# Optimization experiments

Hardware: AMD Instinct MI355X
Metric: run time of the kernel (lower is better)

Reference implementation:

```python
import jax, jax.numpy as jnp
import numpy as np

CHUNK = 64


def _rmsnorm(x, g, eps=1e-6):
    return x * jax.lax.rsqrt(jnp.mean(x * x, axis=-1, keepdims=True) + eps) * g


def setup_inputs() -> dict:
    key = jax.random.key(0)
    ks = jax.random.split(key, 8)
    B, L, D, N = 4, 4096, 512, 64
    s = 0.02
    return {
        'x': jax.random.normal(ks[0], (B, L, D), jnp.float32),
        'A_log': -jnp.ones((D,), jnp.float32) * jnp.log(2.0),
        'dt_bias': jnp.log(jnp.expm1(jax.random.uniform(ks[1], (D,), jnp.float32, 0.001, 0.1))),
        'D_skip': jnp.ones((D,), jnp.float32),
        'W_xproj': jax.random.normal(ks[2], (D, 2 * D), jnp.float32) * s,
        'b_xproj': jnp.zeros((2 * D,), jnp.float32),
        'W_B': jax.random.normal(ks[3], (D, N), jnp.float32) * s,
        'W_C': jax.random.normal(ks[4], (D, N), jnp.float32) * s,
        'W_dt': jax.random.normal(ks[5], (D, D), jnp.float32) * s,
        'g_Bnorm': jnp.ones((N,), jnp.float32),
        'g_Cnorm': jnp.ones((N,), jnp.float32),
        'g_outnorm': jnp.ones((D,), jnp.float32),
        'W_out': jax.random.normal(ks[6], (D, D), jnp.float32) * s,
        'b_out': jnp.zeros((D,), jnp.float32),
    }


def reference(x, A_log, dt_bias, D_skip, W_xproj, b_xproj, W_B, W_C, W_dt,
              g_Bnorm, g_Cnorm, g_outnorm, W_out, b_out):
    b, l, d = x.shape
    n = W_B.shape[1]
    p = CHUNK
    c = l // p  # L chosen divisible by chunk size (original pads otherwise)

    A = -jnp.exp(jnp.clip(A_log, -20.0, 2.0))  # (d,)
    xp = x @ W_xproj + b_xproj                  # (b,l,2d)
    x_bar, z = jnp.split(xp, 2, axis=-1)
    Bm = _rmsnorm(x_bar @ W_B, g_Bnorm)         # (b,l,n)
    Cm = _rmsnorm(x_bar @ W_C, g_Cnorm)         # (b,l,n)
    dt = jnp.clip(jax.nn.softplus(x_bar @ W_dt + dt_bias), 1e-4, 5.0)
    A_bar = jnp.exp(jnp.clip(dt * A, -20.0, 0.0))  # (b,l,d)

    to_chunks = lambda t: t.reshape(b, c, p, t.shape[-1]).transpose(1, 0, 2, 3)
    xc, Bc, Cc, Ac = map(to_chunks, (x_bar, Bm, Cm, A_bar))  # (c,b,p,*)
    mask = jnp.tril(jnp.ones((p, p), x.dtype))

    def process_chunk(prev_state, inputs):
        x_c, B_c, C_c, A_c = inputs
        log_a = jnp.log(jnp.clip(A_c, 1e-8, 1.0))
        la_cs = jnp.cumsum(log_a, axis=1)  # (b,p,d)
        # intra-chunk decay matrix M: (b,p,p,d)
        M = jnp.exp(la_cs[:, :, None, :] - la_cs[:, None, :, :]) * mask[None, :, :, None]
        BX = jnp.einsum('bpn,bpd->bpnd', B_c, x_c)
        state = jnp.einsum('bijd,bjnd->bind', M, BX)
        y_intra = jnp.einsum('bpn,bpnd->bpd', C_c, state)
        decay = jnp.exp(la_cs)
        y_inter = jnp.einsum('bpn,bpnd->bpd', C_c,
                             prev_state[:, None, :, :] * decay[:, :, None, :])
        y_c = y_intra + y_inter
        a_total = jnp.exp(la_cs[:, -1, :])             # (b,d)
        a_to_end = jnp.exp(la_cs[:, -1:, :] - la_cs)   # (b,p,d)
        chunk_state = jnp.einsum('bpn,bpd->bnd', B_c, x_c * a_to_end)
        new_state = prev_state * a_total[:, None, :] + chunk_state
        new_state = jnp.where(jnp.isfinite(new_state), new_state, 0.0)
        y_c = jnp.where(jnp.isfinite(y_c), y_c, 0.0)
        return new_state, y_c

    init = jnp.zeros((b, n, d), x.dtype)
    _, yc = jax.lax.scan(jax.checkpoint(process_chunk), init, (xc, Bc, Cc, Ac))
    y = yc.transpose(1, 0, 2, 3).reshape(b, l, d)
    y = jnp.where(jnp.isfinite(y), y, 0.0)
    y = y + D_skip * x_bar
    y = _rmsnorm(y, g_outnorm) * jax.nn.silu(z)
    return y @ W_out + b_out
```

## Files before the change

kernel.cpp:

```cpp
#include <hip/hip_runtime.h>
#include <hip/hip_bf16.h>
#include <math.h>

typedef __hip_bfloat16 bf16;
typedef __attribute__((ext_vector_type(8))) short short8;
typedef __attribute__((ext_vector_type(4))) float floatx4;

#define B_ 4
#define L_ 4096
#define D_ 512
#define M_ (B_*L_)

__device__ __forceinline__ float b2f(bf16 v){ return __bfloat162float(v); }
__device__ __forceinline__ bf16  f2b(float v){ return __float2bfloat16(v); }
__device__ __forceinline__ short f2bs(float v){ bf16 h = __float2bfloat16(v); short s; __builtin_memcpy(&s,&h,2); return s; }
__device__ __forceinline__ short8 cvt8(float4 a, float4 b){
    short8 s; s[0]=f2bs(a.x); s[1]=f2bs(a.y); s[2]=f2bs(a.z); s[3]=f2bs(a.w);
    s[4]=f2bs(b.x); s[5]=f2bs(b.y); s[6]=f2bs(b.z); s[7]=f2bs(b.w); return s;
}

__global__ __launch_bounds__(1024) void k_transpose(const float* __restrict__ src,
                                                    bf16* __restrict__ dst, int K, int N){
    __shared__ float tile[32][33];
    int n0 = blockIdx.x*32, k0 = blockIdx.y*32;
    int tx = threadIdx.x, ty = threadIdx.y;
    tile[ty][tx] = src[(size_t)(k0+ty)*N + n0+tx];
    __syncthreads();
    ((short*)dst)[(size_t)(n0+ty)*K + k0+tx] = f2bs(tile[tx][ty]);
}

template<int EPI, bool AF32>
__global__ __launch_bounds__(256) void k_gemm128(const void* __restrict__ Ap,
        const bf16* __restrict__ Wt, const float* __restrict__ bias,
        const float* __restrict__ aux,
        float* __restrict__ o1, bf16* __restrict__ o2, bf16* __restrict__ o3){
    __shared__ short As[128][40];
    __shared__ short Bs[128][40];
    const int K = 512;
    int m0 = blockIdx.x*128, n0 = blockIdx.y*128;
    int tid=threadIdx.x, w=tid>>6, lane=tid&63;
    int wr=w>>1, wc=w&1, quad=lane>>4, r16=lane&15;
    floatx4 acc[4][4];
    #pragma unroll
    for (int i=0;i<4;i++)
        #pragma unroll
        for (int j=0;j<4;j++)
            #pragma unroll
            for (int e=0;e<4;e++) acc[i][j][e]=0.f;

    int srow = tid>>1, scg = (tid&1)*16;
    for (int k0=0;k0<K;k0+=32){
        if (AF32){
            const float* ap = (const float*)Ap + (size_t)(m0+srow)*K + k0 + scg;
            float4 a0=*(const float4*)ap, a1=*(const float4*)(ap+4),
                   a2=*(const float4*)(ap+8), a3=*(const float4*)(ap+12);
            *(short8*)&As[srow][scg]   = cvt8(a0,a1);
            *(short8*)&As[srow][scg+8] = cvt8(a2,a3);
        } else {
            const short* ap = (const short*)Ap + (size_t)(m0+srow)*K + k0 + scg;
            *(short8*)&As[srow][scg]   = *(const short8*)ap;
            *(short8*)&As[srow][scg+8] = *(const short8*)(ap+8);
        }
        const short* wp = (const short*)Wt + (size_t)(n0+srow)*K + k0 + scg;
        *(short8*)&Bs[srow][scg]   = *(const short8*)wp;
        *(short8*)&Bs[srow][scg+8] = *(const short8*)(wp+8);
        __syncthreads();
        short8 af[4], bv[4];
        #pragma unroll
        for (int i=0;i<4;i++) af[i] = *(short8*)&As[wr*64+i*16+r16][quad*8];
        #pragma unroll
        for (int j=0;j<4;j++) bv[j] = *(short8*)&Bs[wc*64+j*16+r16][quad*8];
        #pragma unroll
        for (int i=0;i<4;i++)
            #pragma unroll
            for (int j=0;j<4;j++)
                acc[i][j] = __builtin_amdgcn_mfma_f32_16x16x32_bf16(af[i], bv[j], acc[i][j], 0,0,0);
        __syncthreads();
    }
    #pragma unroll
    for (int i=0;i<4;i++)
    #pragma unroll
    for (int j=0;j<4;j++)
    #pragma unroll
    for (int reg=0;reg<4;reg++){
        int gr = m0 + wr*64 + i*16 + quad*4 + reg;
        int gc = n0 + wc*64 + j*16 + r16;
        float v = acc[i][j][reg] + bias[gc];
        if (EPI==0){
            if (gc < 512){
                o1[(size_t)gr*512 + gc] = v;
                o2[(size_t)gr*512 + gc] = f2b(v);
            } else {
                o3[(size_t)gr*512 + (gc-512)] = f2b(v / (1.f + expf(-v)));
            }
        } else if (EPI==1){
            float sp = (v > 15.f) ? v : log1pf(expf(v));
            float dt = fminf(fmaxf(sp, 1e-4f), 5.f);
            float Ad = -expf(fminf(fmaxf(aux[gc], -20.f), 2.f));
            o1[(size_t)gr*512 + gc] = fminf(fmaxf(dt*Ad, -18.420680743952367f), 0.f);
        } else {
            o1[(size_t)gr*512 + gc] = v;
        }
    }
}

__device__ __forceinline__ void gemm_tile_64x64(const bf16* __restrict__ Aptr,
                                                const bf16* __restrict__ Wt,
                                                int K, int m0, int n0,
                                                short (*As)[32], short (*Ns)[32],
                                                floatx4 acc[2][2]){
    int tid  = threadIdx.x;
    int w    = tid >> 6, lane = tid & 63;
    int wr   = w >> 1,  wc   = w & 1;
    int quad = lane >> 4, r16 = lane & 15;
    #pragma unroll
    for (int i=0;i<2;i++)
        #pragma unroll
        for (int j=0;j<2;j++)
            #pragma unroll
            for (int e=0;e<4;e++) acc[i][j][e] = 0.f;
    int lrow = tid >> 2, lkg = (tid & 3) * 8;
    for (int k0 = 0; k0 < K; k0 += 32){
        *(short8*)&As[lrow][lkg] = *(const short8*)((const short*)Aptr + (size_t)(m0+lrow)*K + k0 + lkg);
        *(short8*)&Ns[lrow][lkg] = *(const short8*)((const short*)Wt   + (size_t)(n0+lrow)*K + k0 + lkg);
        __syncthreads();
        short8 af[2], bfr[2];
        #pragma unroll
        for (int t=0;t<2;t++) af[t]  = *(short8*)&As[wr*32 + t*16 + r16][quad*8];
        #pragma unroll
        for (int t=0;t<2;t++) bfr[t] = *(short8*)&Ns[wc*32 + t*16 + r16][quad*8];
        #pragma unroll
        for (int i=0;i<2;i++)
            #pragma unroll
            for (int j=0;j<2;j++)
                acc[i][j] = __builtin_amdgcn_mfma_f32_16x16x32_bf16(af[i], bfr[j], acc[i][j], 0,0,0);
        __syncthreads();
    }
}

__global__ __launch_bounds__(256) void k_bcproj(const bf16* __restrict__ xbarh,
        const bf16* __restrict__ WtB, const bf16* __restrict__ WtC,
        const float* __restrict__ gB, const float* __restrict__ gC,
        float* __restrict__ Bm, float* __restrict__ Cm){
    __shared__ short As[64][32], Ns[64][32];
    __shared__ float Ls[64][64];
    __shared__ float rfac[64];
    const bf16* Wt = blockIdx.y ? WtC : WtB;
    const float* g = blockIdx.y ? gC  : gB;
    float* outp    = blockIdx.y ? Cm  : Bm;
    floatx4 acc[2][2];
    int m0 = blockIdx.x*64;
    gemm_tile_64x64(xbarh, Wt, 512, m0, 0, As, Ns, acc);
    int tid=threadIdx.x, w=tid>>6, lane=tid&63, wr=w>>1, wc=w&1, quad=lane>>4, r16=lane&15;
    #pragma unroll
    for (int i=0;i<2;i++)
    #pragma unroll
    for (int j=0;j<2;j++)
    #pragma unroll
    for (int reg=0;reg<4;reg++)
        Ls[wr*32+i*16+quad*4+reg][wc*32+j*16+r16] = acc[i][j][reg];
    __syncthreads();
    if (tid < 64){
        float ss = 0.f;
        #pragma unroll
        for (int cc=0;cc<64;cc++){ float t = Ls[tid][cc]; ss += t*t; }
        rfac[tid] = rsqrtf(ss*(1.f/64.f) + 1e-6f);
    }
    __syncthreads();
    #pragma unroll
    for (int it=0; it<16; it++){
        int idx = it*256 + tid;
        int r = idx >> 6, cc = idx & 63;
        outp[(size_t)(m0+r)*64 + cc] = Ls[r][cc] * rfac[r] * g[cc];
    }
}

__global__ __launch_bounds__(512) void k_pass1(float* __restrict__ la_dec,
        const float* __restrict__ xbar, const float* __restrict__ Bm,
        const float* __restrict__ Cm, float* __restrict__ ybuf,
        float* __restrict__ local, float* __restrict__ atot){
    int c=blockIdx.x, b=blockIdx.y, d=threadIdx.x;
    size_t rowbase=(size_t)b*L_+(size_t)c*64;
    size_t cb=(size_t)c*4+b;
    float4 st[16];
    #pragma unroll
    for (int k=0;k<16;k++) st[k]=make_float4(0.f,0.f,0.f,0.f);
    float cs=0.f, decv=0.f;
    size_t off0 = rowbase*512 + d;
    float la_n = la_dec[off0], x_n = xbar[off0];
    #pragma unroll 2
    for (int i=0;i<64;i++){
        size_t off=(rowbase+i)*512+d;
        float lai=la_n, xi=x_n;
        if (i<63){ la_n=la_dec[off+512]; x_n=xbar[off+512]; }
        float ai=__expf(lai);
        cs += lai;
        decv=__expf(cs);
        la_dec[off]=decv;
        const float* Br=Bm+(rowbase+i)*64;
        const float* Cr=Cm+(rowbase+i)*64;
        float4 yv=make_float4(0.f,0.f,0.f,0.f);
        #pragma unroll
        for (int k=0;k<16;k++){
            float4 bv=*(const float4*)(Br+k*4);
            float4 cv=*(const float4*)(Cr+k*4);
            float4 s=st[k];
            s.x=fmaf(ai,s.x,bv.x*xi); s.y=fmaf(ai,s.y,bv.y*xi);
            s.z=fmaf(ai,s.z,bv.z*xi); s.w=fmaf(ai,s.w,bv.w*xi);
            st[k]=s;
            yv.x=fmaf(cv.x,s.x,yv.x); yv.y=fmaf(cv.y,s.y,yv.y);
            yv.z=fmaf(cv.z,s.z,yv.z); yv.w=fmaf(cv.w,s.w,yv.w);
        }
        ybuf[off]=(yv.x+yv.y)+(yv.z+yv.w);
    }
    #pragma unroll
    for (int k=0;k<16;k++){
        size_t ob=(cb*64 + k*4)*512 + d;
        local[ob]        = st[k].x;
        local[ob+512]    = st[k].y;
        local[ob+1024]   = st[k].z;
        local[ob+1536]   = st[k].w;
    }
    atot[cb*512+d]=decv;
}

__global__ __launch_bounds__(256) void k_scan(float* __restrict__ local,
        const float* __restrict__ atot){
    int idx = blockIdx.x*256 + threadIdx.x;
    int d = idx & 511, n = (idx >> 9) & 63, b = idx >> 15;
    float s = 0.f;
    for (int c=0;c<64;c++){
        size_t cb = (size_t)c*4 + b;
        size_t off = (cb*64 + n)*512 + d;
        float v = local[off];
        local[off] = s;
        s = s * atot[cb*512 + d] + v;
        if (!isfinite(s)) s = 0.f;
    }
}

__global__ __launch_bounds__(256) void k_inter(const float* __restrict__ Cm,
        const float* __restrict__ Sprev, const float* __restrict__ dec,
        float* __restrict__ ybuf){
    __shared__ short Cs[64][72];
    __shared__ short Ss[64][72];
    int c=blockIdx.x, b=blockIdx.y, d0=blockIdx.z*64;
    size_t rowbase=(size_t)b*L_+(size_t)c*64;
    size_t cb=(size_t)c*4+b;
    int tid=threadIdx.x, w=tid>>6, lane=tid&63;
    int wr=w>>1, wc=w&1, quad=lane>>4, r16=lane&15;
    {
        int row=tid&63, cg=(tid>>6)*16;
        const float* cp=Cm+(rowbase+row)*64+cg;
        float4 c0=*(const float4*)cp, c1=*(const float4*)(cp+4),
               c2=*(const float4*)(cp+8), c3=*(const float4*)(cp+12);
        *(short8*)&Cs[row][cg]   = cvt8(c0,c1);
        *(short8*)&Cs[row][cg+8] = cvt8(c2,c3);
        int n=tid>>2, dg=(tid&3)*16;
        const float* sp=Sprev+(cb*64+n)*512+d0+dg;
        float4 v0=*(const float4*)sp, v1=*(const float4*)(sp+4),
               v2=*(const float4*)(sp+8), v3=*(const float4*)(sp+12);
        Ss[dg+ 0][n]=f2bs(v0.x); Ss[dg+ 1][n]=f2bs(v0.y); Ss[dg+ 2][n]=f2bs(v0.z); Ss[dg+ 3][n]=f2bs(v0.w);
        Ss[dg+ 4][n]=f2bs(v1.x); Ss[dg+ 5][n]=f2bs(v1.y); Ss[dg+ 6][n]=f2bs(v1.z); Ss[dg+ 7][n]=f2bs(v1.w);
        Ss[dg+ 8][n]=f2bs(v2.x); Ss[dg+ 9][n]=f2bs(v2.y); Ss[dg+10][n]=f2bs(v2.z); Ss[dg+11][n]=f2bs(v2.w);
        Ss[dg+12][n]=f2bs(v3.x); Ss[dg+13][n]=f2bs(v3.y); Ss[dg+14][n]=f2bs(v3.z); Ss[dg+15][n]=f2bs(v3.w);
    }
    __syncthreads();
    floatx4 acc[2][2];
    #pragma unroll
    for (int i=0;i<2;i++)
        #pragma unroll
        for (int j=0;j<2;j++)
            #pragma unroll
            for (int e=0;e<4;e++) acc[i][j][e]=0.f;
    #pragma unroll
    for (int ks=0;ks<2;ks++){
        short8 af[2], bv[2];
        #pragma unroll
        for (int i=0;i<2;i++) af[i]=*(short8*)&Cs[wr*32+i*16+r16][ks*32+quad*8];
        #pragma unroll
        for (int j=0;j<2;j++) bv[j]=*(short8*)&Ss[wc*32+j*16+r16][ks*32+quad*8];
        #pragma unroll
        for (int i=0;i<2;i++)
            #pragma unroll
            for (int j=0;j<2;j++)
                acc[i][j]=__builtin_amdgcn_mfma_f32_16x16x32_bf16(af[i],bv[j],acc[i][j],0,0,0);
    }
    #pragma unroll
    for (int i=0;i<2;i++)
    #pragma unroll
    for (int j=0;j<2;j++)
    #pragma unroll
    for (int reg=0;reg<4;reg++){
        int gi = wr*32+i*16+quad*4+reg;
        int gd = d0+wc*32+j*16+r16;
        size_t off=(rowbase+gi)*512+gd;
        ybuf[off]=fmaf(dec[off],acc[i][j][reg],ybuf[off]);
    }
}

__global__ __launch_bounds__(256) void k_outnorm(const float* __restrict__ y,
        const float* __restrict__ xbar, const float* __restrict__ Dskip,
        const float* __restrict__ g, const bf16* __restrict__ siluz,
        bf16* __restrict__ u){
    int wave = threadIdx.x >> 6, lane = threadIdx.x & 63;
    size_t row = (size_t)blockIdx.x*4 + wave;
    float v[8]; float ss = 0.f;
    #pragma unroll
    for (int j=0;j<8;j++){
        int d = j*64 + lane;
        float yv = y[row*512 + d];
        if (!isfinite(yv)) yv = 0.f;
        float t = yv + Dskip[d] * xbar[row*512 + d];
        v[j] = t; ss += t*t;
    }
    #pragma unroll
    for (int m=1;m<64;m<<=1) ss += __shfl_xor(ss, m, 64);
    float r = rsqrtf(ss*(1.f/512.f) + 1e-6f);
    #pragma unroll
    for (int j=0;j<8;j++){
        int d = j*64 + lane;
        u[row*512 + d] = f2b(v[j] * r * g[d] * b2f(siluz[row*512 + d]));
    }
}

extern "C" void kernel_launch(void* const* d_in, const int* in_sizes, int n_in,
                              void* d_out, int out_size, void* d_ws, size_t ws_size,
                              hipStream_t stream){
    const float* x       = (const float*)d_in[0];
    const float* A_log   = (const float*)d_in[1];
    const float* dt_bias = (const float*)d_in[2];
    const float* D_skip  = (const float*)d_in[3];
    const float* W_xproj = (const float*)d_in[4];
    const float* b_xproj = (const float*)d_in[5];
    const float* W_B     = (const float*)d_in[6];
    const float* W_C     = (const float*)d_in[7];
    const float* W_dt    = (const float*)d_in[8];
    const float* g_B     = (const float*)d_in[9];
    const float* g_C     = (const float*)d_in[10];
    const float* g_out   = (const float*)d_in[11];
    const float* W_out   = (const float*)d_in[12];
    const float* b_out   = (const float*)d_in[13];
    float* out = (float*)d_out;

    char* wp = (char*)d_ws;
    auto alloc = [&](size_t bytes)->char*{ char* p = wp; wp += (bytes + 255) & ~(size_t)255; return p; };
    float* xbar  = (float*)alloc((size_t)M_*512*4);
    bf16*  xbarh = (bf16*) alloc((size_t)M_*512*2);
    bf16*  siluz = (bf16*) alloc((size_t)M_*512*2);
    float* la    = (float*)alloc((size_t)M_*512*4);
    float* Bm    = (float*)alloc((size_t)M_*64*4);
    float* Cm    = (float*)alloc((size_t)M_*64*4);
    float* local = (float*)alloc((size_t)256*64*512*4);
    float* atot  = (float*)alloc((size_t)256*512*4);
    float* ybuf  = (float*)alloc((size_t)M_*512*4);
    bf16*  u     = (bf16*) alloc((size_t)M_*512*2);
    bf16*  WtX   = (bf16*) alloc((size_t)1024*512*2);
    bf16*  WtD   = (bf16*) alloc((size_t)512*512*2);
    bf16*  WtO   = (bf16*) alloc((size_t)512*512*2);
    bf16*  WtB   = (bf16*) alloc((size_t)64*512*2);
    bf16*  WtC   = (bf16*) alloc((size_t)64*512*2);

    dim3 tb(32,32);
    k_transpose<<<dim3(32,16), tb, 0, stream>>>(W_xproj, WtX, 512, 1024);
    k_transpose<<<dim3(16,16), tb, 0, stream>>>(W_dt,   WtD, 512, 512);
    k_transpose<<<dim3(16,16), tb, 0, stream>>>(W_out,  WtO, 512, 512);
    k_transpose<<<dim3(2,16),  tb, 0, stream>>>(W_B,    WtB, 512, 64);
    k_transpose<<<dim3(2,16),  tb, 0, stream>>>(W_C,    WtC, 512, 64);

    k_gemm128<0,true> <<<dim3(128, 8), 256, 0, stream>>>(x,     WtX, b_xproj, nullptr, xbar, xbarh, siluz);
    k_bcproj          <<<dim3(256, 2), 256, 0, stream>>>(xbarh, WtB, WtC, g_B, g_C, Bm, Cm);
    k_gemm128<1,false><<<dim3(128, 4), 256, 0, stream>>>(xbarh, WtD, dt_bias, A_log, la, nullptr, nullptr);
    k_pass1           <<<dim3(64, 4),  512, 0, stream>>>(la, xbar, Bm, Cm, ybuf, local, atot);
    k_scan            <<<512,          256, 0, stream>>>(local, atot);
    k_inter           <<<dim3(64,4,8), 256, 0, stream>>>(Cm, local, la, ybuf);
    k_outnorm         <<<M_/4,         256, 0, stream>>>(ybuf, xbar, D_skip, g_out, siluz, u);
    k_gemm128<2,false><<<dim3(128, 4), 256, 0, stream>>>(u,     WtO, b_out, nullptr, out, nullptr, nullptr);
}
```

Measured before the change: 403.7 us.

## Restructure scan into state-only pass1 and recompute pass2; use direct-to-LDS GEMM loads

Several changes land together. The GEMM now loads bf16 tiles straight into LDS with global_load_lds, using unpadded tiles, and the first GEMM gets its input from a separate fp32-to-bf16 conversion kernel instead of converting inside the loop. The chunk scan is split differently: pass1 computes only the chunk-final states, with B staged in shared memory and d split across blocks. A new pass2 starts from the scanned previous state, recomputes the recurrence and writes y directly, which replaces the MFMA inter-chunk kernel and the decay write-back. Precise exp calls in the GEMM epilogues become fast intrinsics. The cost is a second sequential pass over each chunk, an extra conversion kernel with its bf16 buffer, and possible LDS bank conflicts from dropping the padding.

```diff
diff --git a/kernel.cpp b/kernel.cpp
--- a/kernel.cpp
+++ b/kernel.cpp
@@ -14,10 +14,10 @@
 __device__ __forceinline__ float b2f(bf16 v){ return __bfloat162float(v); }
 __device__ __forceinline__ bf16  f2b(float v){ return __float2bfloat16(v); }
 __device__ __forceinline__ short f2bs(float v){ bf16 h = __float2bfloat16(v); short s; __builtin_memcpy(&s,&h,2); return s; }
-__device__ __forceinline__ short8 cvt8(float4 a, float4 b){
-    short8 s; s[0]=f2bs(a.x); s[1]=f2bs(a.y); s[2]=f2bs(a.z); s[3]=f2bs(a.w);
-    s[4]=f2bs(b.x); s[5]=f2bs(b.y); s[6]=f2bs(b.z); s[7]=f2bs(b.w); return s;
-}
+
+#define GLD16(gp, lp) __builtin_amdgcn_global_load_lds( \
+    (const __attribute__((address_space(1))) void*)(gp), \
+    (__attribute__((address_space(3))) void*)(lp), 16, 0, 0)
 
 __global__ __launch_bounds__(1024) void k_transpose(const float* __restrict__ src,
                                                     bf16* __restrict__ dst, int K, int N){
@@ -29,13 +29,21 @@
     ((short*)dst)[(size_t)(n0+ty)*K + k0+tx] = f2bs(tile[tx][ty]);
 }
 
-template<int EPI, bool AF32>
-__global__ __launch_bounds__(256) void k_gemm128(const void* __restrict__ Ap,
+__global__ __launch_bounds__(256) void k_cvt(const float* __restrict__ src,
+                                             bf16* __restrict__ dst){
+    size_t i = ((size_t)blockIdx.x*256 + threadIdx.x)*4;
+    float4 v = *(const float4*)(src + i);
+    short4 s; s.x=f2bs(v.x); s.y=f2bs(v.y); s.z=f2bs(v.z); s.w=f2bs(v.w);
+    *(short4*)((short*)dst + i) = s;
+}
+
+template<int EPI>
+__global__ __launch_bounds__(256) void k_gemm(const bf16* __restrict__ Ap,
         const bf16* __restrict__ Wt, const float* __restrict__ bias,
         const float* __restrict__ aux,
         float* __restrict__ o1, bf16* __restrict__ o2, bf16* __restrict__ o3){
-    __shared__ short As[128][40];
-    __shared__ short Bs[128][40];
+    __shared__ short As[128*32];
+    __shared__ short Bs[128*32];
     const int K = 512;
     int m0 = blockIdx.x*128, n0 = blockIdx.y*128;
     int tid=threadIdx.x, w=tid>>6, lane=tid&63;
@@ -48,28 +56,23 @@
             #pragma unroll
             for (int e=0;e<4;e++) acc[i][j][e]=0.f;
 
-    int srow = tid>>1, scg = (tid&1)*16;
+    int c0 = tid, c1 = tid + 256;
+    const short* Ab = (const short*)Ap + (size_t)m0*K;
+    const short* Wb = (const short*)Wt + (size_t)n0*K;
+    int r0 = c0>>2, g0 = (c0&3)*8;
+    int r1 = c1>>2, g1 = (c1&3)*8;
+
     for (int k0=0;k0<K;k0+=32){
-        if (AF32){
-            const float* ap = (const float*)Ap + (size_t)(m0+srow)*K + k0 + scg;
-            float4 a0=*(const float4*)ap, a1=*(const float4*)(ap+4),
-                   a2=*(const float4*)(ap+8), a3=*(const float4*)(ap+12);
-            *(short8*)&As[srow][scg]   = cvt8(a0,a1);
-            *(short8*)&As[srow][scg+8] = cvt8(a2,a3);
-        } else {
-            const short* ap = (const short*)Ap + (size_t)(m0+srow)*K + k0 + scg;
-            *(short8*)&As[srow][scg]   = *(const short8*)ap;
-            *(short8*)&As[srow][scg+8] = *(const short8*)(ap+8);
-        }
-        const short* wp = (const short*)Wt + (size_t)(n0+srow)*K + k0 + scg;
-        *(short8*)&Bs[srow][scg]   = *(const short8*)wp;
-        *(short8*)&Bs[srow][scg+8] = *(const short8*)(wp+8);
+        GLD16(Ab + (size_t)r0*K + k0 + g0, &As[c0*8]);
+        GLD16(Ab + (size_t)r1*K + k0 + g1, &As[c1*8]);
+        GLD16(Wb + (size_t)r0*K + k0 + g0, &Bs[c0*8]);
+        GLD16(Wb + (size_t)r1*K + k0 + g1, &Bs[c1*8]);
         __syncthreads();
         short8 af[4], bv[4];
         #pragma unroll
-        for (int i=0;i<4;i++) af[i] = *(short8*)&As[wr*64+i*16+r16][quad*8];
-        #pragma unroll
-        for (int j=0;j<4;j++) bv[j] = *(short8*)&Bs[wc*64+j*16+r16][quad*8];
+        for (int i=0;i<4;i++) af[i] = *(short8*)&As[(wr*64+i*16+r16)*32 + quad*8];
+        #pragma unroll
+        for (int j=0;j<4;j++) bv[j] = *(short8*)&Bs[(wc*64+j*16+r16)*32 + quad*8];
         #pragma unroll
         for (int i=0;i<4;i++)
             #pragma unroll
@@ -91,12 +94,12 @@
                 o1[(size_t)gr*512 + gc] = v;
                 o2[(size_t)gr*512 + gc] = f2b(v);
             } else {
-                o3[(size_t)gr*512 + (gc-512)] = f2b(v / (1.f + expf(-v)));
+                o3[(size_t)gr*512 + (gc-512)] = f2b(v / (1.f + __expf(-v)));
             }
         } else if (EPI==1){
-            float sp = (v > 15.f) ? v : log1pf(expf(v));
+            float sp = (v > 15.f) ? v : log1pf(__expf(v));
             float dt = fminf(fmaxf(sp, 1e-4f), 5.f);
-            float Ad = -expf(fminf(fmaxf(aux[gc], -20.f), 2.f));
+            float Ad = -__expf(fminf(fmaxf(aux[gc], -20.f), 2.f));
             o1[(size_t)gr*512 + gc] = fminf(fmaxf(dt*Ad, -18.420680743952367f), 0.f);
         } else {
             o1[(size_t)gr*512 + gc] = v;
@@ -175,53 +178,51 @@
     }
 }
 
-__global__ __launch_bounds__(512) void k_pass1(float* __restrict__ la_dec,
+__global__ __launch_bounds__(256) void k_pass1(const float* __restrict__ la,
         const float* __restrict__ xbar, const float* __restrict__ Bm,
-        const float* __restrict__ Cm, float* __restrict__ ybuf,
         float* __restrict__ local, float* __restrict__ atot){
-    int c=blockIdx.x, b=blockIdx.y, d=threadIdx.x;
+    __shared__ float Bs[64*64];
+    int c=blockIdx.x, b=blockIdx.y, d=blockIdx.z*256+threadIdx.x;
     size_t rowbase=(size_t)b*L_+(size_t)c*64;
     size_t cb=(size_t)c*4+b;
+    {
+        const float4* src=(const float4*)(Bm + rowbase*64);
+        float4* dst=(float4*)Bs;
+        #pragma unroll
+        for (int k=0;k<4;k++) dst[k*256+threadIdx.x]=src[k*256+threadIdx.x];
+    }
+    __syncthreads();
     float4 st[16];
     #pragma unroll
     for (int k=0;k<16;k++) st[k]=make_float4(0.f,0.f,0.f,0.f);
-    float cs=0.f, decv=0.f;
-    size_t off0 = rowbase*512 + d;
-    float la_n = la_dec[off0], x_n = xbar[off0];
+    float cs=0.f;
+    size_t off0=rowbase*512+d;
+    float la_n=la[off0], x_n=xbar[off0];
     #pragma unroll 2
     for (int i=0;i<64;i++){
-        size_t off=(rowbase+i)*512+d;
         float lai=la_n, xi=x_n;
-        if (i<63){ la_n=la_dec[off+512]; x_n=xbar[off+512]; }
+        if (i<63){ la_n=la[off0+(i+1)*512]; x_n=xbar[off0+(i+1)*512]; }
         float ai=__expf(lai);
         cs += lai;
-        decv=__expf(cs);
-        la_dec[off]=decv;
-        const float* Br=Bm+(rowbase+i)*64;
-        const float* Cr=Cm+(rowbase+i)*64;
-        float4 yv=make_float4(0.f,0.f,0.f,0.f);
+        const float* Br=Bs+i*64;
         #pragma unroll
         for (int k=0;k<16;k++){
             float4 bv=*(const float4*)(Br+k*4);
-            float4 cv=*(const float4*)(Cr+k*4);
             float4 s=st[k];
             s.x=fmaf(ai,s.x,bv.x*xi); s.y=fmaf(ai,s.y,bv.y*xi);
             s.z=fmaf(ai,s.z,bv.z*xi); s.w=fmaf(ai,s.w,bv.w*xi);
             st[k]=s;
-            yv.x=fmaf(cv.x,s.x,yv.x); yv.y=fmaf(cv.y,s.y,yv.y);
-            yv.z=fmaf(cv.z,s.z,yv.z); yv.w=fmaf(cv.w,s.w,yv.w);
         }
-        ybuf[off]=(yv.x+yv.y)+(yv.z+yv.w);
     }
     #pragma unroll
     for (int k=0;k<16;k++){
         size_t ob=(cb*64 + k*4)*512 + d;
-        local[ob]        = st[k].x;
-        local[ob+512]    = st[k].y;
-        local[ob+1024]   = st[k].z;
-        local[ob+1536]   = st[k].w;
-    }
-    atot[cb*512+d]=decv;
+        local[ob]      = st[k].x;
+        local[ob+512]  = st[k].y;
+        local[ob+1024] = st[k].z;
+        local[ob+1536] = st[k].w;
+    }
+    atot[cb*512+d]=__expf(cs);
 }
 
 __global__ __launch_bounds__(256) void k_scan(float* __restrict__ local,
@@ -239,63 +240,57 @@
     }
 }
 
-__global__ __launch_bounds__(256) void k_inter(const float* __restrict__ Cm,
-        const float* __restrict__ Sprev, const float* __restrict__ dec,
+__global__ __launch_bounds__(256) void k_pass2(const float* __restrict__ la,
+        const float* __restrict__ xbar, const float* __restrict__ Bm,
+        const float* __restrict__ Cm, const float* __restrict__ Sprev,
         float* __restrict__ ybuf){
-    __shared__ short Cs[64][72];
-    __shared__ short Ss[64][72];
-    int c=blockIdx.x, b=blockIdx.y, d0=blockIdx.z*64;
+    __shared__ float Bs[64*64];
+    __shared__ float Cs[64*64];
+    int c=blockIdx.x, b=blockIdx.y, d=blockIdx.z*256+threadIdx.x;
     size_t rowbase=(size_t)b*L_+(size_t)c*64;
     size_t cb=(size_t)c*4+b;
-    int tid=threadIdx.x, w=tid>>6, lane=tid&63;
-    int wr=w>>1, wc=w&1, quad=lane>>4, r16=lane&15;
     {
-        int row=tid&63, cg=(tid>>6)*16;
-        const float* cp=Cm+(rowbase+row)*64+cg;
-        float4 c0=*(const float4*)cp, c1=*(const float4*)(cp+4),
-               c2=*(const float4*)(cp+8), c3=*(const float4*)(cp+12);
-        *(short8*)&Cs[row][cg]   = cvt8(c0,c1);
-        *(short8*)&Cs[row][cg+8] = cvt8(c2,c3);
-        int n=tid>>2, dg=(tid&3)*16;
-        const float* sp=Sprev+(cb*64+n)*512+d0+dg;
-        float4 v0=*(const float4*)sp, v1=*(const float4*)(sp+4),
-               v2=*(const float4*)(sp+8), v3=*(const float4*)(sp+12);
-        Ss[dg+ 0][n]=f2bs(v0.x); Ss[dg+ 1][n]=f2bs(v0.y); Ss[dg+ 2][n]=f2bs(v0.z); Ss[dg+ 3][n]=f2bs(v0.w);
-        Ss[dg+ 4][n]=f2bs(v1.x); Ss[dg+ 5][n]=f2bs(v1.y); Ss[dg+ 6][n]=f2bs(v1.z); Ss[dg+ 7][n]=f2bs(v1.w);
-        Ss[dg+ 8][n]=f2bs(v2.x); Ss[dg+ 9][n]=f2bs(v2.y); Ss[dg+10][n]=f2bs(v2.z); Ss[dg+11][n]=f2bs(v2.w);
-        Ss[dg+12][n]=f2bs(v3.x); Ss[dg+13][n]=f2bs(v3.y); Ss[dg+14][n]=f2bs(v3.z); Ss[dg+15][n]=f2bs(v3.w);
-    }
-    __syncthreads();
-    floatx4 acc[2][2];
-    #pragma unroll
-    for (int i=0;i<2;i++)
-        #pragma unroll
-        for (int j=0;j<2;j++)
-            #pragma unroll
-            for (int e=0;e<4;e++) acc[i][j][e]=0.f;
-    #pragma unroll
-    for (int ks=0;ks<2;ks++){
-        short8 af[2], bv[2];
-        #pragma unroll
-        for (int i=0;i<2;i++) af[i]=*(short8*)&Cs[wr*32+i*16+r16][ks*32+quad*8];
-        #pragma unroll
-        for (int j=0;j<2;j++) bv[j]=*(short8*)&Ss[wc*32+j*16+r16][ks*32+quad*8];
-        #pragma unroll
-        for (int i=0;i<2;i++)
-            #pragma unroll
-            for (int j=0;j<2;j++)
-                acc[i][j]=__builtin_amdgcn_mfma_f32_16x16x32_bf16(af[i],bv[j],acc[i][j],0,0,0);
-    }
-    #pragma unroll
-    for (int i=0;i<2;i++)
-    #pragma unroll
-    for (int j=0;j<2;j++)
-    #pragma unroll
-    for (int reg=0;reg<4;reg++){
-        int gi = wr*32+i*16+quad*4+reg;
-        int gd = d0+wc*32+j*16+r16;
-        size_t off=(rowbase+gi)*512+gd;
-        ybuf[off]=fmaf(dec[off],acc[i][j][reg],ybuf[off]);
+        const float4* sb=(const float4*)(Bm + rowbase*64);
+        const float4* sc=(const float4*)(Cm + rowbase*64);
+        float4* db=(float4*)Bs; float4* dc=(float4*)Cs;
+        #pragma unroll
+        for (int k=0;k<4;k++){
+            db[k*256+threadIdx.x]=sb[k*256+threadIdx.x];
+            dc[k*256+threadIdx.x]=sc[k*256+threadIdx.x];
+        }
+    }
+    float4 st[16];
+    #pragma unroll
+    for (int k=0;k<16;k++){
+        size_t ib=(cb*64 + k*4)*512 + d;
+        st[k].x=Sprev[ib]; st[k].y=Sprev[ib+512];
+        st[k].z=Sprev[ib+1024]; st[k].w=Sprev[ib+1536];
+    }
+    __syncthreads();
+    size_t off0=rowbase*512+d;
+    float la_n=la[off0], x_n=xbar[off0];
+    #pragma unroll 2
+    for (int i=0;i<64;i++){
+        float lai=la_n, xi=x_n;
+        if (i<63){ la_n=la[off0+(i+1)*512]; x_n=xbar[off0+(i+1)*512]; }
+        float ai=__expf(lai);
+        const float* Br=Bs+i*64;
+        const float* Cr=Cs+i*64;
+        float4 yv=make_float4(0.f,0.f,0.f,0.f);
+        #pragma unroll
+        for (int k=0;k<16;k++){
+            float4 bv=*(const float4*)(Br+k*4);
+            float4 cv=*(const float4*)(Cr+k*4);
+            float4 s=st[k];
+            s.x=fmaf(ai,s.x,bv.x*xi); s.y=fmaf(ai,s.y,bv.y*xi);
+            s.z=fmaf(ai,s.z,bv.z*xi); s.w=fmaf(ai,s.w,bv.w*xi);
+            st[k]=s;
+            yv.x=fmaf(cv.x,s.x,yv.x); yv.y=fmaf(cv.y,s.y,yv.y);
+            yv.z=fmaf(cv.z,s.z,yv.z); yv.w=fmaf(cv.w,s.w,yv.w);
+        }
+        float yo=(yv.x+yv.y)+(yv.z+yv.w);
+        if (!isfinite(yo)) yo=0.f;
+        ybuf[off0+i*512]=yo;
     }
 }
 
@@ -309,9 +304,7 @@
     #pragma unroll
     for (int j=0;j<8;j++){
         int d = j*64 + lane;
-        float yv = y[row*512 + d];
-        if (!isfinite(yv)) yv = 0.f;
-        float t = yv + Dskip[d] * xbar[row*512 + d];
+        float t = y[row*512 + d] + Dskip[d] * xbar[row*512 + d];
         v[j] = t; ss += t*t;
     }
     #pragma unroll
@@ -346,6 +339,7 @@
     char* wp = (char*)d_ws;
     auto alloc = [&](size_t bytes)->char*{ char* p = wp; wp += (bytes + 255) & ~(size_t)255; return p; };
     float* xbar  = (float*)alloc((size_t)M_*512*4);
+    bf16*  xh    = (bf16*) alloc((size_t)M_*512*2);
     bf16*  xbarh = (bf16*) alloc((size_t)M_*512*2);
     bf16*  siluz = (bf16*) alloc((size_t)M_*512*2);
     float* la    = (float*)alloc((size_t)M_*512*4);
@@ -367,13 +361,14 @@
     k_transpose<<<dim3(16,16), tb, 0, stream>>>(W_out,  WtO, 512, 512);
     k_transpose<<<dim3(2,16),  tb, 0, stream>>>(W_B,    WtB, 512, 64);
     k_transpose<<<dim3(2,16),  tb, 0, stream>>>(W_C,    WtC, 512, 64);
-
-    k_gemm128<0,true> <<<dim3(128, 8), 256, 0, stream>>>(x,     WtX, b_xproj, nullptr, xbar, xbarh, siluz);
-    k_bcproj          <<<dim3(256, 2), 256, 0, stream>>>(xbarh, WtB, WtC, g_B, g_C, Bm, Cm);
-    k_gemm128<1,false><<<dim3(128, 4), 256, 0, stream>>>(xbarh, WtD, dt_bias, A_log, la, nullptr, nullptr);
-    k_pass1           <<<dim3(64, 4),  512, 0, stream>>>(la, xbar, Bm, Cm, ybuf, local, atot);
-    k_scan            <<<512,          256, 0, stream>>>(local, atot);
-    k_inter           <<<dim3(64,4,8), 256, 0, stream>>>(Cm, local, la, ybuf);
-    k_outnorm         <<<M_/4,         256, 0, stream>>>(ybuf, xbar, D_skip, g_out, siluz, u);
-    k_gemm128<2,false><<<dim3(128, 4), 256, 0, stream>>>(u,     WtO, b_out, nullptr, out, nullptr, nullptr);
-}
+    k_cvt      <<<M_*512/1024, 256, 0, stream>>>(x, xh);
+
+    k_gemm<0> <<<dim3(128, 8), 256, 0, stream>>>(xh,    WtX, b_xproj, nullptr, xbar, xbarh, siluz);
+    k_bcproj  <<<dim3(256, 2), 256, 0, stream>>>(xbarh, WtB, WtC, g_B, g_C, Bm, Cm);
+    k_gemm<1> <<<dim3(128, 4), 256, 0, stream>>>(xbarh, WtD, dt_bias, A_log, la, nullptr, nullptr);
+    k_pass1   <<<dim3(64,4,2), 256, 0, stream>>>(la, xbar, Bm, local, atot);
+    k_scan    <<<512,          256, 0, stream>>>(local, atot);
+    k_pass2   <<<dim3(64,4,2), 256, 0, stream>>>(la, xbar, Bm, Cm, local, ybuf);
+    k_outnorm <<<M_/4,         256, 0, stream>>>(ybuf, xbar, D_skip, g_out, siluz, u);
+    k_gemm<2> <<<dim3(128, 4), 256, 0, stream>>>(u,     WtO, b_out, nullptr, out, nullptr, nullptr);
+}
```

After: 372.4 us. 1.08x faster.
